# Kernel optimization log

Measured on AMD Instinct MI355X. Metric: run time of the kernel, lower is better.

Reference implementation:

```python
import jax, jax.numpy as jnp
import numpy as np

B, S, C, HD = 1, 2048, 2048, 128
H = C // HD  # 16 heads
EPS = float(jnp.finfo(jnp.float32).eps)  # torch nn.RMSNorm default eps


def setup_inputs() -> dict:
    key = jax.random.key(0)
    ks = jax.random.split(key, 10)
    std = 1.0 / np.sqrt(C)
    return {
        "x": jax.random.normal(ks[0], (B, S, C), jnp.float32),
        "rope": jax.random.normal(ks[1], (1, S, 1, HD // 2, 2, 2), jnp.float32),
        "wq": jax.random.normal(ks[2], (C, C), jnp.float32) * std,
        "bq": jax.random.normal(ks[3], (C,), jnp.float32) * 0.01,
        "wk": jax.random.normal(ks[4], (C, C), jnp.float32) * std,
        "bk": jax.random.normal(ks[5], (C,), jnp.float32) * 0.01,
        "wv": jax.random.normal(ks[6], (C, C), jnp.float32) * std,
        "bv": jax.random.normal(ks[7], (C,), jnp.float32) * 0.01,
        "q_norm_w": jnp.ones((HD,), jnp.float32),
        "k_norm_w": jnp.ones((HD,), jnp.float32),
        "wo": jax.random.normal(ks[8], (C, C), jnp.float32) * std,
        "bo": jax.random.normal(ks[9], (C,), jnp.float32) * 0.01,
    }


def _rmsnorm(x, w):
    # x: [..., HD]
    ms = jnp.mean(x * x, axis=-1, keepdims=True)
    return x * jax.lax.rsqrt(ms + EPS) * w


def _apply_rotary(x, rope):
    # x: [B,S,H,HD]; rope: [1,S,1,HD//2,2,2]
    shp = x.shape
    x_ = x.reshape(*shp[:-1], -1, 1, 2)          # [B,S,H,HD/2,1,2]
    out = (rope * x_).sum(axis=-1)               # [B,S,H,HD/2,2]
    return out.reshape(shp)


def reference(x, rope, wq, bq, wk, bk, wv, bv, q_norm_w, k_norm_w, wo, bo):
    q = x @ wq.T + bq
    k = x @ wk.T + bk
    v = x @ wv.T + bv
    q = q.reshape(B, S, H, HD)
    k = k.reshape(B, S, H, HD)
    v = v.reshape(B, S, H, HD)
    q = _rmsnorm(q, q_norm_w)
    k = _rmsnorm(k, k_norm_w)
    q = _apply_rotary(q, rope)
    k = _apply_rotary(k, rope)
    scale = 1.0 / np.sqrt(HD)
    scores = jnp.einsum("bqhd,bkhd->bhqk", q, k) * scale  # [B,H,S,S]
    attn = jax.nn.softmax(scores, axis=-1)
    out = jnp.einsum("bhqk,bkhd->bqhd", attn, v).reshape(B, S, C)
    return out @ wo.T + bo
```

## Files before the change

kernel.cpp:

```cpp
#include <hip/hip_runtime.h>
#include <stdint.h>

#define GLOBAL_AS __attribute__((address_space(1)))
#define LDS_AS    __attribute__((address_space(3)))

typedef unsigned short u16;
typedef __attribute__((ext_vector_type(8))) __bf16 bf16x8;
typedef __attribute__((ext_vector_type(4))) float   f32x4;
typedef __attribute__((ext_vector_type(2))) float   f32x2;
typedef __attribute__((ext_vector_type(4))) u16     u16x4;

#if __has_builtin(__builtin_amdgcn_exp2f)
#define EXP2(x) __builtin_amdgcn_exp2f(x)
#else
#define EXP2(x) __exp2f(x)
#endif

static __device__ __forceinline__ float bf2f(u16 u) {
    union { uint32_t i; float f; } c; c.i = ((uint32_t)u) << 16; return c.f;
}
static __device__ __forceinline__ u16 f2bf(float f) {
    union { float f; uint32_t i; } c; c.f = f;
    uint32_t r = c.i + 0x7fffu + ((c.i >> 16) & 1u);
    return (u16)(r >> 16);
}
static __device__ __forceinline__ u16 f2bf_fast(float f) {
    union { float f; uint32_t i; } c; c.f = f;
    return (u16)((c.i + 0x8000u) >> 16);
}
static __device__ __forceinline__ void gl_lds16(const void* g, void* l) {
    __builtin_amdgcn_global_load_lds((GLOBAL_AS const uint32_t*)g,
                                     (LDS_AS uint32_t*)l, 16, 0, 0);
}
static __device__ __forceinline__ f32x4 mfma16(bf16x8 a, bf16x8 b, f32x4 c) {
    return __builtin_amdgcn_mfma_f32_16x16x32_bf16(a, b, c, 0, 0, 0);
}

__global__ __launch_bounds__(256) void cast5(
    const float* __restrict__ s0, const float* __restrict__ s1,
    const float* __restrict__ s2, const float* __restrict__ s3,
    const float* __restrict__ s4,
    u16* __restrict__ d0, u16* __restrict__ d1, u16* __restrict__ d2,
    u16* __restrict__ d3, u16* __restrict__ d4)
{
    const float* s; u16* d;
    switch (blockIdx.y) {
        case 0: s = s0; d = d0; break;
        case 1: s = s1; d = d1; break;
        case 2: s = s2; d = d2; break;
        case 3: s = s3; d = d3; break;
        default: s = s4; d = d4; break;
    }
    int i = (blockIdx.x * 256 + threadIdx.x) * 4;
    f32x4 v = *(const f32x4*)&s[i];
    u16x4 u = { f2bf(v[0]), f2bf(v[1]), f2bf(v[2]), f2bf(v[3]) };
    *(u16x4*)&d[i] = u;
}

static __device__ __forceinline__ void stage32(const u16* __restrict__ gbase, int k0,
                                               u16* lds, int tid)
{
#pragma unroll
    for (int i = 0; i < 2; ++i) {
        int row = i * 128 + (tid >> 2);
        gl_lds16(gbase + (size_t)row * 2048 + k0 + (tid & 3) * 8,
                 lds + i * 4096 + tid * 8);
    }
}

__global__ __launch_bounds__(512, 2) void gemm_qkv2(
    const u16* __restrict__ x,
    const u16* __restrict__ wq, const u16* __restrict__ wk, const u16* __restrict__ wv,
    const float* __restrict__ bq, const float* __restrict__ bk, const float* __restrict__ bv,
    u16* __restrict__ q, u16* __restrict__ k, u16* __restrict__ v)
{
    __shared__ u16 SL[4][2][8192];
    const int tid = threadIdx.x, l = tid & 63, w = tid >> 6;
    const int wm = w >> 2, wn = w & 3;
    const int lr = l & 15, lg = l >> 4;
    const int bid = blockIdx.x;
    const int bm = bid & 7, bn = bid >> 3;
    const int wsel = bn >> 3, bnl = bn & 7;
    const u16* W = (wsel == 0) ? wq : (wsel == 1) ? wk : wv;
    const float* bias = (wsel == 0) ? bq : (wsel == 1) ? bk : bv;
    u16* C = (wsel == 0) ? q : (wsel == 1) ? k : v;

    const u16* Ab = x + (size_t)(bm * 256) * 2048;
    const u16* Bb = W + (size_t)(bnl * 256) * 2048;

    f32x4 acc[8][4];
#pragma unroll
    for (int mi = 0; mi < 8; ++mi)
#pragma unroll
        for (int nj = 0; nj < 4; ++nj) acc[mi][nj] = (f32x4){0.f, 0.f, 0.f, 0.f};

#pragma unroll
    for (int t = 0; t < 3; ++t) {
        stage32(Ab, t * 32, (u16*)SL[t][0], tid);
        stage32(Bb, t * 32, (u16*)SL[t][1], tid);
    }

    const int arow = wm * 128 + lr;
    const int brow = wn * 64 + lr;

#pragma unroll 1
    for (int t = 0; t < 64; ++t) {
        const u16* As = (const u16*)SL[t & 3][0];
        const u16* Bs = (const u16*)SL[t & 3][1];
        const int tn = (t + 3 < 64) ? (t + 3) : 63;
        u16* SnA = (u16*)SL[(t + 3) & 3][0];
        u16* SnB = (u16*)SL[(t + 3) & 3][1];

        asm volatile("s_waitcnt vmcnt(8)" ::: "memory");
        __builtin_amdgcn_s_barrier();
        __builtin_amdgcn_sched_barrier(0);

        bf16x8 a0[4], b0[4];
#pragma unroll
        for (int mi = 0; mi < 4; ++mi)
            a0[mi] = *(const bf16x8*)&As[(arow + mi * 16) * 32 + lg * 8];
#pragma unroll
        for (int nj = 0; nj < 4; ++nj)
            b0[nj] = *(const bf16x8*)&Bs[(brow + nj * 16) * 32 + lg * 8];
        stage32(Ab, tn * 32, SnA, tid);
        __builtin_amdgcn_s_setprio(1);
#pragma unroll
        for (int mi = 0; mi < 4; ++mi)
#pragma unroll
            for (int nj = 0; nj < 4; ++nj)
                acc[mi][nj] = mfma16(a0[mi], b0[nj], acc[mi][nj]);
        __builtin_amdgcn_s_setprio(0);
        __builtin_amdgcn_s_barrier();
        __builtin_amdgcn_sched_barrier(0);

        bf16x8 a1[4];
#pragma unroll
        for (int mi = 0; mi < 4; ++mi)
            a1[mi] = *(const bf16x8*)&As[(arow + (4 + mi) * 16) * 32 + lg * 8];
        stage32(Bb, tn * 32, SnB, tid);
        __builtin_amdgcn_s_setprio(1);
#pragma unroll
        for (int mi = 0; mi < 4; ++mi)
#pragma unroll
            for (int nj = 0; nj < 4; ++nj)
                acc[4 + mi][nj] = mfma16(a1[mi], b0[nj], acc[4 + mi][nj]);
        __builtin_amdgcn_s_setprio(0);
    }
    asm volatile("s_waitcnt vmcnt(0)" ::: "memory");

#pragma unroll
    for (int mi = 0; mi < 8; ++mi) {
        int row0 = bm * 256 + wm * 128 + mi * 16 + lg * 4;
#pragma unroll
        for (int nj = 0; nj < 4; ++nj) {
            int col = bnl * 256 + wn * 64 + nj * 16 + lr;
            float bs = bias[col];
#pragma unroll
            for (int reg = 0; reg < 4; ++reg)
                C[(size_t)(row0 + reg) * 2048 + col] = f2bf(acc[mi][nj][reg] + bs);
        }
    }
}

template<bool OUT_BF16>
static __device__ __forceinline__ void gemm_body(
    const u16* __restrict__ A, const u16* __restrict__ B,
    const float* __restrict__ bias, void* __restrict__ Cout)
{
    constexpr int K = 2048, N = 2048;
    __shared__ u16 As[128 * 64];
    __shared__ u16 Bs[128 * 64];
    const int tid = threadIdx.x;
    const int l = tid & 63, w = tid >> 6;
    const int wm = w >> 1, wn = w & 1;
    const int lr = l & 15, lg = l >> 4;
    const int bm = blockIdx.x, bn = blockIdx.y;

    f32x4 acc[4][4];
#pragma unroll
    for (int mi = 0; mi < 4; ++mi)
#pragma unroll
        for (int nj = 0; nj < 4; ++nj) acc[mi][nj] = (f32x4){0.f, 0.f, 0.f, 0.f};

    const u16* Ab = A + (size_t)(bm * 128) * K;
    const u16* Bb = B + (size_t)(bn * 128) * K;
    const int srow = (l >> 3);
    const int scol = (l & 7) * 8;

    for (int k0 = 0; k0 < K; k0 += 64) {
        __syncthreads();
#pragma unroll
        for (int r = 0; r < 4; ++r) {
            int c = w * 4 + r;
            int row = c * 8 + srow;
            gl_lds16(Ab + (size_t)row * K + k0 + scol, &As[c * 512 + l * 8]);
            gl_lds16(Bb + (size_t)row * K + k0 + scol, &Bs[c * 512 + l * 8]);
        }
        __syncthreads();
#pragma unroll
        for (int kk = 0; kk < 2; ++kk) {
            bf16x8 a[4], b[4];
#pragma unroll
            for (int mi = 0; mi < 4; ++mi)
                a[mi] = *(const bf16x8*)&As[(wm * 64 + mi * 16 + lr) * 64 + kk * 32 + lg * 8];
#pragma unroll
            for (int nj = 0; nj < 4; ++nj)
                b[nj] = *(const bf16x8*)&Bs[(wn * 64 + nj * 16 + lr) * 64 + kk * 32 + lg * 8];
#pragma unroll
            for (int mi = 0; mi < 4; ++mi)
#pragma unroll
                for (int nj = 0; nj < 4; ++nj)
                    acc[mi][nj] = mfma16(a[mi], b[nj], acc[mi][nj]);
        }
    }
#pragma unroll
    for (int mi = 0; mi < 4; ++mi) {
        int row0 = bm * 128 + wm * 64 + mi * 16 + lg * 4;
#pragma unroll
        for (int nj = 0; nj < 4; ++nj) {
            int col = bn * 128 + wn * 64 + nj * 16 + lr;
            float bs = bias[col];
#pragma unroll
            for (int reg = 0; reg < 4; ++reg) {
                float v = acc[mi][nj][reg] + bs;
                if (OUT_BF16)
                    ((u16*)Cout)[(size_t)(row0 + reg) * N + col] = f2bf(v);
                else
                    ((float*)Cout)[(size_t)(row0 + reg) * N + col] = v;
            }
        }
    }
}

__global__ __launch_bounds__(256) void gemm_outp(
    const u16* __restrict__ a, const u16* __restrict__ wo,
    const float* __restrict__ bo, float* __restrict__ out)
{
    gemm_body<false>(a, wo, bo, out);
}

__global__ __launch_bounds__(256) void norm_rope(
    const u16* __restrict__ qb, const u16* __restrict__ kb,
    const float* __restrict__ rope, const float* __restrict__ qw, const float* __restrict__ kw,
    u16* __restrict__ qh, u16* __restrict__ kh)
{
    const int tid = threadIdx.x, l = tid & 63, w = tid >> 6;
    const int rowid = blockIdx.x * 4 + w;
    const int h = rowid & 15, s = rowid >> 4;
    const size_t gbase = (size_t)s * 2048 + h * 128 + 2 * l;

    uint32_t qu = *(const uint32_t*)&qb[gbase];
    uint32_t ku = *(const uint32_t*)&kb[gbase];
    float q0 = bf2f((u16)qu), q1 = bf2f((u16)(qu >> 16));
    float k0 = bf2f((u16)ku), k1 = bf2f((u16)(ku >> 16));

    float sq = q0 * q0 + q1 * q1;
    float sk = k0 * k0 + k1 * k1;
#pragma unroll
    for (int m = 1; m < 64; m <<= 1) {
        sq += __shfl_xor(sq, m);
        sk += __shfl_xor(sk, m);
    }
    const float EPS = 1.1920928955078125e-07f;
    const float SCALE = 0.08838834764831845f * 1.4426950408889634f;
    float rq = rsqrtf(sq * (1.f / 128.f) + EPS) * SCALE;
    float rk = rsqrtf(sk * (1.f / 128.f) + EPS);

    f32x2 wq2 = *(const f32x2*)&qw[2 * l];
    f32x2 wk2 = *(const f32x2*)&kw[2 * l];
    float qn0 = q0 * rq * wq2[0], qn1 = q1 * rq * wq2[1];
    float kn0 = k0 * rk * wk2[0], kn1 = k1 * rk * wk2[1];

    f32x4 rr = *(const f32x4*)&rope[(size_t)s * 256 + l * 4];
    float qo0 = rr[0] * qn0 + rr[1] * qn1;
    float qo1 = rr[2] * qn0 + rr[3] * qn1;
    float ko0 = rr[0] * kn0 + rr[1] * kn1;
    float ko1 = rr[2] * kn0 + rr[3] * kn1;

    const size_t obase = ((size_t)h * 2048 + s) * 128 + 2 * l;
    *(uint32_t*)&qh[obase] = (uint32_t)f2bf(qo0) | ((uint32_t)f2bf(qo1) << 16);
    *(uint32_t*)&kh[obase] = (uint32_t)f2bf(ko0) | ((uint32_t)f2bf(ko1) << 16);
}

__global__ __launch_bounds__(256) void transpose_v(
    const u16* __restrict__ vb, u16* __restrict__ vt)
{
    __shared__ u16 t[64 * 80];
    const int h = blockIdx.z, s0 = blockIdx.x * 64, d0 = blockIdx.y * 64;
    const int tid = threadIdx.x;
#pragma unroll
    for (int cc = tid; cc < 512; cc += 256) {
        int r = cc >> 3, u = cc & 7;
        *(bf16x8*)&t[r * 80 + u * 8] =
            *(const bf16x8*)&vb[(size_t)(s0 + r) * 2048 + h * 128 + d0 + u * 8];
    }
    __syncthreads();
#pragma unroll
    for (int cc = tid; cc < 512; cc += 256) {
        int dr = cc >> 3, u = cc & 7;
        u16 vv[8];
#pragma unroll
        for (int j = 0; j < 8; ++j) vv[j] = t[(u * 8 + j) * 80 + dr];
        u16x4 lo = { vv[0], vv[1], vv[2], vv[3] };
        u16x4 hi = { vv[4], vv[5], vv[6], vv[7] };
        u16* dst = &vt[((size_t)h * 128 + d0 + dr) * 2048 + s0 + u * 8];
        *(u16x4*)dst = lo;
        *(u16x4*)(dst + 4) = hi;
    }
}

__global__ __launch_bounds__(256, 2) void attn(
    const u16* __restrict__ qh, const u16* __restrict__ kh,
    const u16* __restrict__ vt, float* __restrict__ Op, float* __restrict__ Lp)
{
    __shared__ u16 Ks[64 * 128];
    __shared__ u16 Vs[128 * 64];
    __shared__ u16 Ps[4][32 * 68];
    const int tid = threadIdx.x, l = tid & 63, w = tid >> 6;
    const int h = blockIdx.z, half = blockIdx.y;
    const int q0 = blockIdx.x * 128 + w * 32;
    const int lr = l & 15, lg = l >> 4;
    const float SHIFT = -17.312340490667562f;

    const u16* Kh = kh + (size_t)h * 2048 * 128;
    const u16* Vh = vt + (size_t)h * 128 * 2048;
    const int kvbase = half * 1024;

    bf16x8 qf[2][4];
#pragma unroll
    for (int am = 0; am < 2; ++am)
#pragma unroll
        for (int kk = 0; kk < 4; ++kk)
            qf[am][kk] = *(const bf16x8*)
                &qh[((size_t)h * 2048 + q0 + am * 16 + lr) * 128 + kk * 32 + lg * 8];

    bf16x8 onesf;
#pragma unroll
    for (int j = 0; j < 8; ++j) {
        union { u16 u; __bf16 b; } cb; cb.u = 0x3F80;
        onesf[j] = cb.b;
    }

    f32x4 o[2][8];
#pragma unroll
    for (int am = 0; am < 2; ++am)
#pragma unroll
        for (int dj = 0; dj < 8; ++dj) o[am][dj] = (f32x4){0.f, 0.f, 0.f, 0.f};
    f32x4 ol[2] = { (f32x4){0.f, 0.f, 0.f, 0.f}, (f32x4){0.f, 0.f, 0.f, 0.f} };

#pragma unroll 1
    for (int t = 0; t < 16; ++t) {
        const int kv0 = kvbase + t * 64;
        __syncthreads();
#pragma unroll
        for (int r = 0; r < 4; ++r) {
            int c = w * 4 + r;
            {
                int row = c * 4 + (l >> 4);
                int u = (l & 15) ^ (row & 7);
                gl_lds16(Kh + (size_t)(kv0 + row) * 128 + u * 8, &Ks[c * 512 + l * 8]);
            }
            {
                int row = c * 8 + (l >> 3);
                int u = (l & 7) ^ (row & 7);
                gl_lds16(Vh + (size_t)row * 2048 + kv0 + u * 8, &Vs[c * 512 + l * 8]);
            }
        }
        __syncthreads();

        f32x4 sc[2][4];
#pragma unroll
        for (int am = 0; am < 2; ++am)
#pragma unroll
            for (int nj = 0; nj < 4; ++nj)
                sc[am][nj] = (f32x4){SHIFT, SHIFT, SHIFT, SHIFT};
        __builtin_amdgcn_s_setprio(1);
#pragma unroll
        for (int kk = 0; kk < 4; ++kk)
#pragma unroll
            for (int nj = 0; nj < 4; ++nj) {
                int n = nj * 16 + lr;
                bf16x8 b = *(const bf16x8*)&Ks[n * 128 + ((kk * 4 + lg) ^ (n & 7)) * 8];
#pragma unroll
                for (int am = 0; am < 2; ++am)
                    sc[am][nj] = mfma16(qf[am][kk], b, sc[am][nj]);
            }
        __builtin_amdgcn_s_setprio(0);

#pragma unroll
        for (int am = 0; am < 2; ++am)
#pragma unroll
            for (int reg = 0; reg < 4; ++reg)
#pragma unroll
                for (int nj = 0; nj < 4; ++nj)
                    Ps[w][(am * 16 + lg * 4 + reg) * 68 + nj * 16 + lr] =
                        f2bf_fast(EXP2(sc[am][nj][reg]));
        asm volatile("s_waitcnt lgkmcnt(0)" ::: "memory");
        __builtin_amdgcn_sched_barrier(0);

        bf16x8 pa[2][2];
#pragma unroll
        for (int am = 0; am < 2; ++am)
#pragma unroll
            for (int kk2 = 0; kk2 < 2; ++kk2) {
                union { u16x4 h4[2]; bf16x8 v8; } cvt;
                cvt.h4[0] = *(const u16x4*)&Ps[w][(am * 16 + lr) * 68 + kk2 * 32 + lg * 8];
                cvt.h4[1] = *(const u16x4*)&Ps[w][(am * 16 + lr) * 68 + kk2 * 32 + lg * 8 + 4];
                pa[am][kk2] = cvt.v8;
            }
        __builtin_amdgcn_s_setprio(1);
#pragma unroll
        for (int am = 0; am < 2; ++am)
#pragma unroll
            for (int kk2 = 0; kk2 < 2; ++kk2)
                ol[am] = mfma16(pa[am][kk2], onesf, ol[am]);
#pragma unroll
        for (int dj = 0; dj < 8; ++dj)
#pragma unroll
            for (int kk2 = 0; kk2 < 2; ++kk2) {
                int n = dj * 16 + lr;
                bf16x8 b = *(const bf16x8*)&Vs[n * 64 + ((kk2 * 4 + lg) ^ (n & 7)) * 8];
#pragma unroll
                for (int am = 0; am < 2; ++am)
                    o[am][dj] = mfma16(pa[am][kk2], b, o[am][dj]);
            }
        __builtin_amdgcn_s_setprio(0);
    }

    if (lr == 0) {
#pragma unroll
        for (int am = 0; am < 2; ++am)
#pragma unroll
            for (int reg = 0; reg < 4; ++reg)
                Lp[(half * 16 + h) * 2048 + q0 + am * 16 + lg * 4 + reg] = ol[am][reg];
    }
#pragma unroll
    for (int am = 0; am < 2; ++am)
#pragma unroll
        for (int dj = 0; dj < 8; ++dj)
#pragma unroll
            for (int reg = 0; reg < 4; ++reg)
                Op[((size_t)half * 2048 + q0 + am * 16 + lg * 4 + reg) * 2048 +
                   h * 128 + dj * 16 + lr] = o[am][dj][reg];
}

__global__ __launch_bounds__(256) void combine(
    const float* __restrict__ Op, const float* __restrict__ Lp, u16* __restrict__ ab)
{
    int idx = (blockIdx.x * 256 + threadIdx.x) * 4;
    int s = idx >> 11, c = idx & 2047, h = c >> 7;
    f32x4 a = *(const f32x4*)&Op[(size_t)s * 2048 + c];
    f32x4 b = *(const f32x4*)&Op[(size_t)(2048 + s) * 2048 + c];
    float rl = 1.0f / (Lp[h * 2048 + s] + Lp[(16 + h) * 2048 + s]);
    u16x4 u = { f2bf((a[0] + b[0]) * rl), f2bf((a[1] + b[1]) * rl),
                f2bf((a[2] + b[2]) * rl), f2bf((a[3] + b[3]) * rl) };
    *(u16x4*)&ab[idx] = u;
}

extern "C" void kernel_launch(void* const* d_in, const int* in_sizes, int n_in,
                              void* d_out, int out_size, void* d_ws, size_t ws_size,
                              hipStream_t stream)
{
    (void)in_sizes; (void)n_in; (void)out_size;
    const float* x    = (const float*)d_in[0];
    const float* rope = (const float*)d_in[1];
    const float* wq   = (const float*)d_in[2];
    const float* bq   = (const float*)d_in[3];
    const float* wk   = (const float*)d_in[4];
    const float* bk   = (const float*)d_in[5];
    const float* wv   = (const float*)d_in[6];
    const float* bv   = (const float*)d_in[7];
    const float* qw   = (const float*)d_in[8];
    const float* kw   = (const float*)d_in[9];
    const float* wo   = (const float*)d_in[10];
    const float* bo   = (const float*)d_in[11];
    float* out = (float*)d_out;

    const size_t NE = 2048ull * 2048ull;
    if (ws_size < 13 * NE * 2) return;
    u16* p = (u16*)d_ws;
    u16* xb  = p; p += NE;
    u16* wqb = p; p += NE;
    u16* wkb = p; p += NE;
    u16* wvb = p; p += NE;
    u16* wob = p; p += NE;
    u16* qb  = p; p += NE;
    u16* kb  = p; p += NE;
    u16* vb  = p; p += NE;
    u16* qhb = p; p += NE;
    u16* khb = p; p += NE;
    u16* vhb = p; p += NE;
    u16* vtb = p; p += NE;
    u16* ab  = p; p += NE;
    (void)vhb;

    float* Op = (float*)xb;
    float* Lp = (float*)qb;

    cast5<<<dim3(4096, 5), 256, 0, stream>>>(x, wq, wk, wv, wo, xb, wqb, wkb, wvb, wob);
    gemm_qkv2<<<192, 512, 0, stream>>>(xb, wqb, wkb, wvb, bq, bk, bv, qb, kb, vb);
    norm_rope<<<8192, 256, 0, stream>>>(qb, kb, rope, qw, kw, qhb, khb);
    transpose_v<<<dim3(32, 2, 16), 256, 0, stream>>>(vb, vtb);
    attn<<<dim3(16, 2, 16), 256, 0, stream>>>(qhb, khb, vtb, Op, Lp);
    combine<<<4096, 256, 0, stream>>>(Op, Lp, ab);
    gemm_outp<<<dim3(16, 16), 256, 0, stream>>>(ab, wob, bo, out);
}
```

Measured before the change: 189.5 us.

## Retile QKV GEMM to 256x192 tiles and pipeline output projection GEMM

The QKV projection moves from 192 blocks of 256x256 tiles to 256 blocks of 256x192 tiles that span the concatenated wq/wk/wv rows. This fills all 256 CUs in a single wave and issues the whole prefetch up front in each iteration. The output projection is rewritten from a synchronous 128x128 K=64 loop into a 512-thread kernel with a 4-stage async global-to-LDS pipeline and XCD-aware block mapping. The cost is smaller per-block arithmetic intensity, extra per-column selection logic in the QKV epilogue, and more waves per tile in the output GEMM.

```diff
diff --git a/kernel.cpp b/kernel.cpp
--- a/kernel.cpp
+++ b/kernel.cpp
@@ -57,186 +57,180 @@
     *(u16x4*)&d[i] = u;
 }
 
-static __device__ __forceinline__ void stage32(const u16* __restrict__ gbase, int k0,
-                                               u16* lds, int tid)
-{
-#pragma unroll
-    for (int i = 0; i < 2; ++i) {
-        int row = i * 128 + (tid >> 2);
-        gl_lds16(gbase + (size_t)row * 2048 + k0 + (tid & 3) * 8,
-                 lds + i * 4096 + tid * 8);
-    }
-}
-
-__global__ __launch_bounds__(512, 2) void gemm_qkv2(
+static __device__ __forceinline__ void stage_qkv(
+    const u16* __restrict__ Ab,
+    const u16* __restrict__ wq, const u16* __restrict__ wk, const u16* __restrict__ wv,
+    int bn, int k0, u16* slot, int tid)
+{
+#pragma unroll
+    for (int i = 0; i < 4; ++i) {
+        int unit = i * 512 + tid;
+        const u16* src;
+        if (i < 2) {
+            int row = unit >> 2, c = unit & 3;
+            src = Ab + (size_t)row * 2048 + k0 + c * 8;
+        } else {
+            int ub = unit - 1024; if (ub > 767) ub = 767;
+            int row = ub >> 2, c = ub & 3;
+            int gr = bn * 192 + row;
+            const u16* base = gr < 2048 ? wq : (gr < 4096 ? wk : wv);
+            src = base + (size_t)(gr & 2047) * 2048 + k0 + c * 8;
+        }
+        gl_lds16(src, slot + unit * 8);
+    }
+}
+
+__global__ __launch_bounds__(512, 2) void gemm_qkv3(
     const u16* __restrict__ x,
     const u16* __restrict__ wq, const u16* __restrict__ wk, const u16* __restrict__ wv,
     const float* __restrict__ bq, const float* __restrict__ bk, const float* __restrict__ bv,
     u16* __restrict__ q, u16* __restrict__ k, u16* __restrict__ v)
 {
-    __shared__ u16 SL[4][2][8192];
+    __shared__ u16 SL[4][16384];
     const int tid = threadIdx.x, l = tid & 63, w = tid >> 6;
     const int wm = w >> 2, wn = w & 3;
     const int lr = l & 15, lg = l >> 4;
     const int bid = blockIdx.x;
     const int bm = bid & 7, bn = bid >> 3;
-    const int wsel = bn >> 3, bnl = bn & 7;
-    const u16* W = (wsel == 0) ? wq : (wsel == 1) ? wk : wv;
-    const float* bias = (wsel == 0) ? bq : (wsel == 1) ? bk : bv;
-    u16* C = (wsel == 0) ? q : (wsel == 1) ? k : v;
 
     const u16* Ab = x + (size_t)(bm * 256) * 2048;
-    const u16* Bb = W + (size_t)(bnl * 256) * 2048;
-
-    f32x4 acc[8][4];
+
+    f32x4 acc[8][3];
 #pragma unroll
     for (int mi = 0; mi < 8; ++mi)
 #pragma unroll
-        for (int nj = 0; nj < 4; ++nj) acc[mi][nj] = (f32x4){0.f, 0.f, 0.f, 0.f};
-
-#pragma unroll
-    for (int t = 0; t < 3; ++t) {
-        stage32(Ab, t * 32, (u16*)SL[t][0], tid);
-        stage32(Bb, t * 32, (u16*)SL[t][1], tid);
-    }
-
-    const int arow = wm * 128 + lr;
-    const int brow = wn * 64 + lr;
+        for (int nj = 0; nj < 3; ++nj) acc[mi][nj] = (f32x4){0.f, 0.f, 0.f, 0.f};
+
+#pragma unroll
+    for (int t = 0; t < 3; ++t)
+        stage_qkv(Ab, wq, wk, wv, bn, t * 32, (u16*)SL[t], tid);
 
 #pragma unroll 1
     for (int t = 0; t < 64; ++t) {
-        const u16* As = (const u16*)SL[t & 3][0];
-        const u16* Bs = (const u16*)SL[t & 3][1];
-        const int tn = (t + 3 < 64) ? (t + 3) : 63;
-        u16* SnA = (u16*)SL[(t + 3) & 3][0];
-        u16* SnB = (u16*)SL[(t + 3) & 3][1];
+        const u16* As = (const u16*)SL[t & 3];
+        const u16* Bs = As + 8192;
+        const int tn = (t + 3 <= 63) ? (t + 3) : 63;
 
         asm volatile("s_waitcnt vmcnt(8)" ::: "memory");
         __builtin_amdgcn_s_barrier();
         __builtin_amdgcn_sched_barrier(0);
 
-        bf16x8 a0[4], b0[4];
-#pragma unroll
-        for (int mi = 0; mi < 4; ++mi)
-            a0[mi] = *(const bf16x8*)&As[(arow + mi * 16) * 32 + lg * 8];
-#pragma unroll
-        for (int nj = 0; nj < 4; ++nj)
-            b0[nj] = *(const bf16x8*)&Bs[(brow + nj * 16) * 32 + lg * 8];
-        stage32(Ab, tn * 32, SnA, tid);
+        stage_qkv(Ab, wq, wk, wv, bn, tn * 32, (u16*)SL[(t + 3) & 3], tid);
+
+        bf16x8 a[8], b[3];
+#pragma unroll
+        for (int mi = 0; mi < 8; ++mi)
+            a[mi] = *(const bf16x8*)&As[(wm * 128 + mi * 16 + lr) * 32 + lg * 8];
+#pragma unroll
+        for (int nj = 0; nj < 3; ++nj)
+            b[nj] = *(const bf16x8*)&Bs[(wn * 48 + nj * 16 + lr) * 32 + lg * 8];
         __builtin_amdgcn_s_setprio(1);
 #pragma unroll
-        for (int mi = 0; mi < 4; ++mi)
-#pragma unroll
-            for (int nj = 0; nj < 4; ++nj)
-                acc[mi][nj] = mfma16(a0[mi], b0[nj], acc[mi][nj]);
+        for (int mi = 0; mi < 8; ++mi)
+#pragma unroll
+            for (int nj = 0; nj < 3; ++nj)
+                acc[mi][nj] = mfma16(a[mi], b[nj], acc[mi][nj]);
         __builtin_amdgcn_s_setprio(0);
+    }
+    asm volatile("s_waitcnt vmcnt(0)" ::: "memory");
+
+#pragma unroll
+    for (int mi = 0; mi < 8; ++mi) {
+        int row0 = bm * 256 + wm * 128 + mi * 16 + lg * 4;
+#pragma unroll
+        for (int nj = 0; nj < 3; ++nj) {
+            int col = bn * 192 + wn * 48 + nj * 16 + lr;
+            int cs = (col >> 11), cc = col & 2047;
+            u16* C = cs == 0 ? q : (cs == 1 ? k : v);
+            const float* bp = cs == 0 ? bq : (cs == 1 ? bk : bv);
+            float bs = bp[cc];
+#pragma unroll
+            for (int reg = 0; reg < 4; ++reg)
+                C[(size_t)(row0 + reg) * 2048 + cc] = f2bf(acc[mi][nj][reg] + bs);
+        }
+    }
+}
+
+static __device__ __forceinline__ void stage_out(
+    const u16* __restrict__ Ab, const u16* __restrict__ Bb,
+    int k0, u16* slot, int tid)
+{
+    {
+        int row = tid >> 2, c = tid & 3;
+        gl_lds16(Ab + (size_t)row * 2048 + k0 + c * 8, slot + tid * 8);
+    }
+    {
+        int row = tid >> 2, c = tid & 3;
+        gl_lds16(Bb + (size_t)row * 2048 + k0 + c * 8, slot + 4096 + tid * 8);
+    }
+}
+
+__global__ __launch_bounds__(512, 2) void gemm_out2(
+    const u16* __restrict__ a, const u16* __restrict__ wo,
+    const float* __restrict__ bo, float* __restrict__ out)
+{
+    __shared__ u16 SL[4][8192];
+    const int tid = threadIdx.x, l = tid & 63, w = tid >> 6;
+    const int wm = w >> 2, wn = w & 3;
+    const int lr = l & 15, lg = l >> 4;
+    const int bid = blockIdx.x;
+    const int xcd = bid & 7, j = bid >> 3;
+    const int bm = xcd * 2 + (j & 1), bn = j >> 1;
+
+    const u16* Ab = a  + (size_t)(bm * 128) * 2048;
+    const u16* Bb = wo + (size_t)(bn * 128) * 2048;
+
+    f32x4 acc[4][2];
+#pragma unroll
+    for (int mi = 0; mi < 4; ++mi)
+#pragma unroll
+        for (int nj = 0; nj < 2; ++nj) acc[mi][nj] = (f32x4){0.f, 0.f, 0.f, 0.f};
+
+#pragma unroll
+    for (int t = 0; t < 3; ++t)
+        stage_out(Ab, Bb, t * 32, (u16*)SL[t], tid);
+
+#pragma unroll 1
+    for (int t = 0; t < 64; ++t) {
+        const u16* As = (const u16*)SL[t & 3];
+        const u16* Bs = As + 4096;
+        const int tn = (t + 3 <= 63) ? (t + 3) : 63;
+
+        asm volatile("s_waitcnt vmcnt(4)" ::: "memory");
         __builtin_amdgcn_s_barrier();
         __builtin_amdgcn_sched_barrier(0);
 
-        bf16x8 a1[4];
+        stage_out(Ab, Bb, tn * 32, (u16*)SL[(t + 3) & 3], tid);
+
+        bf16x8 af[4], bf[2];
 #pragma unroll
         for (int mi = 0; mi < 4; ++mi)
-            a1[mi] = *(const bf16x8*)&As[(arow + (4 + mi) * 16) * 32 + lg * 8];
-        stage32(Bb, tn * 32, SnB, tid);
+            af[mi] = *(const bf16x8*)&As[(wm * 64 + mi * 16 + lr) * 32 + lg * 8];
+#pragma unroll
+        for (int nj = 0; nj < 2; ++nj)
+            bf[nj] = *(const bf16x8*)&Bs[(wn * 32 + nj * 16 + lr) * 32 + lg * 8];
         __builtin_amdgcn_s_setprio(1);
 #pragma unroll
         for (int mi = 0; mi < 4; ++mi)
 #pragma unroll
-            for (int nj = 0; nj < 4; ++nj)
-                acc[4 + mi][nj] = mfma16(a1[mi], b0[nj], acc[4 + mi][nj]);
+            for (int nj = 0; nj < 2; ++nj)
+                acc[mi][nj] = mfma16(af[mi], bf[nj], acc[mi][nj]);
         __builtin_amdgcn_s_setprio(0);
     }
     asm volatile("s_waitcnt vmcnt(0)" ::: "memory");
 
-#pragma unroll
-    for (int mi = 0; mi < 8; ++mi) {
-        int row0 = bm * 256 + wm * 128 + mi * 16 + lg * 4;
-#pragma unroll
-        for (int nj = 0; nj < 4; ++nj) {
-            int col = bnl * 256 + wn * 64 + nj * 16 + lr;
-            float bs = bias[col];
-#pragma unroll
-            for (int reg = 0; reg < 4; ++reg)
-                C[(size_t)(row0 + reg) * 2048 + col] = f2bf(acc[mi][nj][reg] + bs);
-        }
-    }
-}
-
-template<bool OUT_BF16>
-static __device__ __forceinline__ void gemm_body(
-    const u16* __restrict__ A, const u16* __restrict__ B,
-    const float* __restrict__ bias, void* __restrict__ Cout)
-{
-    constexpr int K = 2048, N = 2048;
-    __shared__ u16 As[128 * 64];
-    __shared__ u16 Bs[128 * 64];
-    const int tid = threadIdx.x;
-    const int l = tid & 63, w = tid >> 6;
-    const int wm = w >> 1, wn = w & 1;
-    const int lr = l & 15, lg = l >> 4;
-    const int bm = blockIdx.x, bn = blockIdx.y;
-
-    f32x4 acc[4][4];
-#pragma unroll
-    for (int mi = 0; mi < 4; ++mi)
-#pragma unroll
-        for (int nj = 0; nj < 4; ++nj) acc[mi][nj] = (f32x4){0.f, 0.f, 0.f, 0.f};
-
-    const u16* Ab = A + (size_t)(bm * 128) * K;
-    const u16* Bb = B + (size_t)(bn * 128) * K;
-    const int srow = (l >> 3);
-    const int scol = (l & 7) * 8;
-
-    for (int k0 = 0; k0 < K; k0 += 64) {
-        __syncthreads();
-#pragma unroll
-        for (int r = 0; r < 4; ++r) {
-            int c = w * 4 + r;
-            int row = c * 8 + srow;
-            gl_lds16(Ab + (size_t)row * K + k0 + scol, &As[c * 512 + l * 8]);
-            gl_lds16(Bb + (size_t)row * K + k0 + scol, &Bs[c * 512 + l * 8]);
-        }
-        __syncthreads();
-#pragma unroll
-        for (int kk = 0; kk < 2; ++kk) {
-            bf16x8 a[4], b[4];
-#pragma unroll
-            for (int mi = 0; mi < 4; ++mi)
-                a[mi] = *(const bf16x8*)&As[(wm * 64 + mi * 16 + lr) * 64 + kk * 32 + lg * 8];
-#pragma unroll
-            for (int nj = 0; nj < 4; ++nj)
-                b[nj] = *(const bf16x8*)&Bs[(wn * 64 + nj * 16 + lr) * 64 + kk * 32 + lg * 8];
-#pragma unroll
-            for (int mi = 0; mi < 4; ++mi)
-#pragma unroll
-                for (int nj = 0; nj < 4; ++nj)
-                    acc[mi][nj] = mfma16(a[mi], b[nj], acc[mi][nj]);
-        }
-    }
 #pragma unroll
     for (int mi = 0; mi < 4; ++mi) {
         int row0 = bm * 128 + wm * 64 + mi * 16 + lg * 4;
 #pragma unroll
-        for (int nj = 0; nj < 4; ++nj) {
-            int col = bn * 128 + wn * 64 + nj * 16 + lr;
-            float bs = bias[col];
-#pragma unroll
-            for (int reg = 0; reg < 4; ++reg) {
-                float v = acc[mi][nj][reg] + bs;
-                if (OUT_BF16)
-                    ((u16*)Cout)[(size_t)(row0 + reg) * N + col] = f2bf(v);
-                else
-                    ((float*)Cout)[(size_t)(row0 + reg) * N + col] = v;
-            }
+        for (int nj = 0; nj < 2; ++nj) {
+            int col = bn * 128 + wn * 32 + nj * 16 + lr;
+            float bs = bo[col];
+#pragma unroll
+            for (int reg = 0; reg < 4; ++reg)
+                out[(size_t)(row0 + reg) * 2048 + col] = acc[mi][nj][reg] + bs;
         }
     }
-}
-
-__global__ __launch_bounds__(256) void gemm_outp(
-    const u16* __restrict__ a, const u16* __restrict__ wo,
-    const float* __restrict__ bo, float* __restrict__ out)
-{
-    gemm_body<false>(a, wo, bo, out);
 }
 
 __global__ __launch_bounds__(256) void norm_rope(
@@ -498,10 +492,10 @@
     float* Lp = (float*)qb;
 
     cast5<<<dim3(4096, 5), 256, 0, stream>>>(x, wq, wk, wv, wo, xb, wqb, wkb, wvb, wob);
-    gemm_qkv2<<<192, 512, 0, stream>>>(xb, wqb, wkb, wvb, bq, bk, bv, qb, kb, vb);
+    gemm_qkv3<<<256, 512, 0, stream>>>(xb, wqb, wkb, wvb, bq, bk, bv, qb, kb, vb);
     norm_rope<<<8192, 256, 0, stream>>>(qb, kb, rope, qw, kw, qhb, khb);
     transpose_v<<<dim3(32, 2, 16), 256, 0, stream>>>(vb, vtb);
     attn<<<dim3(16, 2, 16), 256, 0, stream>>>(qhb, khb, vtb, Op, Lp);
     combine<<<4096, 256, 0, stream>>>(Op, Lp, ab);
-    gemm_outp<<<dim3(16, 16), 256, 0, stream>>>(ab, wob, bo, out);
-}
+    gemm_out2<<<256, 512, 0, stream>>>(ab, wob, bo, out);
+}
```

Measured after the change: 170.3 us. 10.1% less time.
